# Kernel tuning notes

Measured on AMD Instinct MI355X. Metric: run time of the kernel, lower is better.

The kernel has to match this reference:

```python
import jax, jax.numpy as jnp
import numpy as np

B, T, IN, HID, NC = 1024, 128, 512, 1024, 10

def setup_inputs() -> dict:
    key = jax.random.key(0)
    ks = jax.random.split(key, 4)
    x = jax.random.normal(ks[0], (B, T, IN), dtype=jnp.float32)
    Wxh = jax.random.normal(ks[1], (IN, HID), dtype=jnp.float32) * (1.0 / np.sqrt(IN))
    b_xh = jnp.zeros((HID,), dtype=jnp.float32)
    Whh = jax.random.normal(ks[2], (HID, HID), dtype=jnp.float32) * (1.0 / np.sqrt(HID))
    b_hh = jnp.zeros((HID,), dtype=jnp.float32)
    Why = jax.random.normal(ks[3], (HID, NC), dtype=jnp.float32) * (1.0 / np.sqrt(HID))
    b_y = jnp.zeros((NC,), dtype=jnp.float32)
    return {"x": x, "Wxh": Wxh, "b_xh": b_xh, "Whh": Whh, "b_hh": b_hh, "Why": Why, "b_y": b_y}

def reference(x, Wxh, b_xh, Whh, b_hh, Why, b_y):
    # Precompute input projections for all timesteps in one big GEMM: [B,T,HID]
    xproj = jnp.einsum('bti,ih->bth', x, Wxh) + b_xh
    h0 = jnp.zeros((x.shape[0], Whh.shape[0]), dtype=x.dtype)
    def step(h, xp_t):
        h = jnp.tanh(xp_t + h @ Whh + b_hh)
        return h, None
    hT, _ = jax.lax.scan(step, h0, jnp.swapaxes(xproj, 0, 1))  # scan over T
    return hT @ Why + b_y
```

## Files before the change

### kernel.cpp

```cpp
#include <hip/hip_runtime.h>
#include <hip/hip_bf16.h>

#define TT    128
#define BATCH 1024
#define INDIM 512
#define HIDD  1024
#define NCLS  10

typedef __bf16 bf16x8 __attribute__((ext_vector_type(8)));
typedef float  f32x4  __attribute__((ext_vector_type(4)));
typedef unsigned short u16x8 __attribute__((ext_vector_type(8)));

__device__ __forceinline__ unsigned short bf16b(float f) {
    __hip_bfloat16 h = __float2bfloat16(f);
    return __builtin_bit_cast(unsigned short, h);
}

__device__ __forceinline__ float tanh_fast(float x) {
    float e = __expf(2.0f * x);
    return 1.0f - 2.0f * __builtin_amdgcn_rcpf(e + 1.0f);
}

#define WAITV(n) asm volatile("s_waitcnt vmcnt(" #n ")" ::: "memory")
#define BAR()    asm volatile("s_barrier" ::: "memory")

__global__ __launch_bounds__(256) void prep_kernel(
    const float* __restrict__ Whh, const float* __restrict__ Wxh,
    __hip_bfloat16* __restrict__ WhhT_hi, __hip_bfloat16* __restrict__ WhhT_lo,
    __hip_bfloat16* __restrict__ WxhT_hi, __hip_bfloat16* __restrict__ WxhT_lo)
{
    __shared__ float tl[64][68];
    int bid = blockIdx.x, tid = threadIdx.x;
    const float* src; int N, k0, n0, dstride;
    __hip_bfloat16 *dhi, *dlo;
    if (bid < 256) { src = Whh; N = 1024; k0 = (bid >> 4) << 6; n0 = (bid & 15) << 6;
                     dhi = WhhT_hi; dlo = WhhT_lo; dstride = 1024; }
    else { int b = bid - 256; src = Wxh; N = 1024; k0 = (b >> 4) << 6; n0 = (b & 15) << 6;
           dhi = WxhT_hi; dlo = WxhT_lo; dstride = 512; }

    int r = tid >> 2, c0 = (tid & 3) << 4;
    const float* s = src + (size_t)(k0 + r) * N + n0 + c0;
#pragma unroll
    for (int j = 0; j < 4; ++j)
        *(float4*)&tl[r][c0 + j * 4] = *(const float4*)(s + j * 4);
    __syncthreads();

    int rn = tid >> 2, ck0 = (tid & 3) << 4;
    u16x8 hi0, hi1, lo0, lo1;
#pragma unroll
    for (int j = 0; j < 16; ++j) {
        float w = tl[ck0 + j][rn];
        unsigned short hb = bf16b(w);
        float hf = __bfloat162float(__builtin_bit_cast(__hip_bfloat16, hb));
        unsigned short lb = bf16b(w - hf);
        if (j < 8) { hi0[j] = hb; lo0[j] = lb; }
        else       { hi1[j - 8] = hb; lo1[j - 8] = lb; }
    }
    size_t o = (size_t)(n0 + rn) * dstride + k0 + ck0;
    *(u16x8*)(void*)(dhi + o)     = hi0;
    *(u16x8*)(void*)(dhi + o + 8) = hi1;
    *(u16x8*)(void*)(dlo + o)     = lo0;
    *(u16x8*)(void*)(dlo + o + 8) = lo1;
}

__global__ __launch_bounds__(256) void convx_all_kernel(
    const float* __restrict__ x, __hip_bfloat16* __restrict__ xs)
{
    size_t gid = (size_t)blockIdx.x * 256 + threadIdx.x;
    int i  = (int)(gid & 63) << 3;
    size_t bt = gid >> 6;
    int t = (int)(bt & 127);
    int b = (int)(bt >> 7);
    const float* s = x + ((size_t)b * TT + t) * INDIM + i;
    float4 a0 = *(const float4*)s, a1 = *(const float4*)(s + 4);
    u16x8 o;
    o[0]=bf16b(a0.x); o[1]=bf16b(a0.y); o[2]=bf16b(a0.z); o[3]=bf16b(a0.w);
    o[4]=bf16b(a1.x); o[5]=bf16b(a1.y); o[6]=bf16b(a1.z); o[7]=bf16b(a1.w);
    *(u16x8*)(void*)(xs + ((size_t)t * BATCH + b) * INDIM + i) = o;
}

__global__ __launch_bounds__(256) void zero_kernel(
    __hip_bfloat16* __restrict__ h, unsigned* __restrict__ bar)
{
    if (blockIdx.x < 512) {
        size_t i = ((size_t)blockIdx.x * 256 + threadIdx.x) << 3;
        u16x8 z = {0,0,0,0,0,0,0,0};
        *(u16x8*)(void*)(h + i) = z;
    } else {
        uint4 z = {0,0,0,0};
#pragma unroll
        for (int k = 0; k < 8; ++k)
            ((uint4*)bar)[k * 256 + threadIdx.x] = z;
    }
}

#define FRAGA(_b, m, ks) \
    (*(const bf16x8*)((_b) + ((((m)<<4)+ar) << 8) + ((((((ks)<<2)+kg)) ^ (ar & 7)) << 4)))

#define STAGE(basePtr, rs, bufidx, AUX) do {                                   \
    _Pragma("unroll")                                                          \
    for (int _i = 0; _i < 4; ++_i) {                                           \
        int _r = (_i << 4) + (tid >> 4);                                       \
        int _s = (tid & 15) ^ (_r & 7);                                        \
        const void* _g = (const void*)((basePtr) + (size_t)_r * (rs) + (_s << 3)); \
        void* _l = (void*)(smem + ((bufidx) << 14) + (_i << 12) + (wave << 10));   \
        __builtin_amdgcn_global_load_lds(                                      \
            (const __attribute__((address_space(1))) void*)_g,                 \
            (__attribute__((address_space(3))) void*)_l, 16, 0, AUX);          \
    } } while (0)

#define DO_CHUNK(B_ARR, q, bufidx) do {                                        \
    const char* _b = smem + ((bufidx) << 14);                                  \
    _Pragma("unroll")                                                          \
    for (int ks = 0; ks < 4; ++ks) {                                           \
        bf16x8 a0 = FRAGA(_b, 0, ks), a1 = FRAGA(_b, 1, ks);                   \
        bf16x8 a2 = FRAGA(_b, 2, ks), a3 = FRAGA(_b, 3, ks);                   \
        bf16x8 bh = B_ARR[(q)*8+ks*2+0], bl = B_ARR[(q)*8+ks*2+1];             \
        acc0 = __builtin_amdgcn_mfma_f32_16x16x32_bf16(a0, bh, acc0, 0,0,0);   \
        acc1 = __builtin_amdgcn_mfma_f32_16x16x32_bf16(a1, bh, acc1, 0,0,0);   \
        acc2 = __builtin_amdgcn_mfma_f32_16x16x32_bf16(a2, bh, acc2, 0,0,0);   \
        acc3 = __builtin_amdgcn_mfma_f32_16x16x32_bf16(a3, bh, acc3, 0,0,0);   \
        acc0 = __builtin_amdgcn_mfma_f32_16x16x32_bf16(a0, bl, acc0, 0,0,0);   \
        acc1 = __builtin_amdgcn_mfma_f32_16x16x32_bf16(a1, bl, acc1, 0,0,0);   \
        acc2 = __builtin_amdgcn_mfma_f32_16x16x32_bf16(a2, bl, acc2, 0,0,0);   \
        acc3 = __builtin_amdgcn_mfma_f32_16x16x32_bf16(a3, bl, acc3, 0,0,0);   \
    } } while (0)

__global__ __launch_bounds__(256, 1) void rnn_kernel(
    __hip_bfloat16* __restrict__ h0, __hip_bfloat16* __restrict__ h1,
    const __hip_bfloat16* __restrict__ xs,
    const __hip_bfloat16* __restrict__ WhhT_hi, const __hip_bfloat16* __restrict__ WhhT_lo,
    const __hip_bfloat16* __restrict__ WxhT_hi, const __hip_bfloat16* __restrict__ WxhT_lo,
    const float* __restrict__ b_xh, const float* __restrict__ b_hh,
    unsigned* __restrict__ bar)
{
    __shared__ char smem[131072];
    int tid = threadIdx.x, bid = blockIdx.x;
    int by = (bid & 7) | (((bid >> 3) & 1) << 3);
    int bx = bid >> 4;
    int lane = tid & 63, wave = tid >> 6;
    int ar = lane & 15, kg = lane >> 4;
    int wcol = (bx << 6) + (wave << 4);
    int by64 = by << 6;

    bf16x8 Bh[64], Bx[32];
    {
        const __hip_bfloat16* hiB = WhhT_hi + (size_t)(wcol + ar) * HIDD + (kg << 3);
        const __hip_bfloat16* loB = WhhT_lo + (size_t)(wcol + ar) * HIDD + (kg << 3);
#pragma unroll
        for (int c = 0; c < 8; ++c)
#pragma unroll
            for (int ks = 0; ks < 4; ++ks) {
                Bh[c*8 + ks*2 + 0] = *(const bf16x8*)(hiB + c*128 + ks*32);
                Bh[c*8 + ks*2 + 1] = *(const bf16x8*)(loB + c*128 + ks*32);
            }
        const __hip_bfloat16* hiX = WxhT_hi + (size_t)(wcol + ar) * INDIM + (kg << 3);
        const __hip_bfloat16* loX = WxhT_lo + (size_t)(wcol + ar) * INDIM + (kg << 3);
#pragma unroll
        for (int c = 0; c < 4; ++c)
#pragma unroll
            for (int ks = 0; ks < 4; ++ks) {
                Bx[c*8 + ks*2 + 0] = *(const bf16x8*)(hiX + c*128 + ks*32);
                Bx[c*8 + ks*2 + 1] = *(const bf16x8*)(loX + c*128 + ks*32);
            }
    }
    int mycol = wcol + ar;
    float bias = b_xh[mycol] + b_hh[mycol];

    unsigned* grpflags = bar + (by << 9);
    unsigned* myflag   = grpflags + (bx << 5);

    {
        const __hip_bfloat16* xA0 = xs + (size_t)by64 * INDIM;
        STAGE(xA0 + 0*128, INDIM, 2, 0);
        STAGE(xA0 + 1*128, INDIM, 3, 0);
        STAGE(xA0 + 2*128, INDIM, 0, 0);
        STAGE(xA0 + 3*128, INDIM, 1, 0);
    }
    WAITV(0); BAR();

    for (int t = 0; t < TT; ++t) {
        const __hip_bfloat16* hA = (t & 1) ? h1 : h0;
        __hip_bfloat16*       hB = (t & 1) ? h0 : h1;
        const __hip_bfloat16* hR = hA + (size_t)by64 * HIDD;
        const __hip_bfloat16* xN = xs + (size_t)(t + 1) * (BATCH * INDIM)
                                      + (size_t)by64 * INDIM;
        int nl = (t < TT - 1);

        f32x4 acc0 = {0,0,0,0}, acc1 = {0,0,0,0}, acc2 = {0,0,0,0}, acc3 = {0,0,0,0};

        DO_CHUNK(Bx, 0, 2);
        DO_CHUNK(Bx, 1, 3);
        DO_CHUNK(Bx, 2, 0);
        DO_CHUNK(Bx, 3, 1);

        if (t > 0) {
            if (wave == 0) {
                unsigned tgt = (unsigned)t;
                for (;;) {
                    unsigned v = tgt;
                    if (lane < 16)
                        v = __hip_atomic_load(grpflags + (lane << 5), __ATOMIC_RELAXED,
                                              __HIP_MEMORY_SCOPE_SYSTEM);
                    if (__all(v >= tgt)) break;
                    __builtin_amdgcn_s_sleep(1);
                }
            }
        }
        BAR();

        STAGE(hR + 0*128, HIDD, 4, 1);
        STAGE(hR + 1*128, HIDD, 5, 1);
        STAGE(hR + 2*128, HIDD, 6, 1);
        STAGE(hR + 3*128, HIDD, 7, 1);
        STAGE(hR + 4*128, HIDD, 0, 1);
        STAGE(hR + 5*128, HIDD, 1, 1);
        if (nl) {
            STAGE(xN + 0*128, INDIM, 2, 0);
            STAGE(xN + 1*128, INDIM, 3, 0);
            WAITV(16);
        } else {
            WAITV(8);
        }
        BAR();
        DO_CHUNK(Bh, 0, 4);
        DO_CHUNK(Bh, 1, 5);
        DO_CHUNK(Bh, 2, 6);
        DO_CHUNK(Bh, 3, 7);
        if (nl) { WAITV(8); } else { WAITV(0); }
        BAR();
        STAGE(hR + 6*128, HIDD, 6, 1);
        STAGE(hR + 7*128, HIDD, 7, 1);
        DO_CHUNK(Bh, 4, 0);
        DO_CHUNK(Bh, 5, 1);
        WAITV(0);
        BAR();
        if (nl) {
            STAGE(xN + 2*128, INDIM, 0, 0);
            STAGE(xN + 3*128, INDIM, 1, 0);
        }
        DO_CHUNK(Bh, 6, 6);
        DO_CHUNK(Bh, 7, 7);

#pragma unroll
        for (int m = 0; m < 4; ++m) {
            f32x4 a = (m == 0) ? acc0 : (m == 1) ? acc1 : (m == 2) ? acc2 : acc3;
#pragma unroll
            for (int j = 0; j < 4; ++j) {
                int row = by64 + (m << 4) + (kg << 2) + j;
                float v = tanh_fast(a[j] + bias);
                hB[(size_t)row * HIDD + mycol] = __float2bfloat16(v);
            }
        }
        WAITV(0);
        BAR();
        if (nl && tid == 0)
            __hip_atomic_store(myflag, (unsigned)(t + 1), __ATOMIC_RELAXED,
                               __HIP_MEMORY_SCOPE_SYSTEM);
    }
}

__global__ __launch_bounds__(64) void out_kernel(
    const __hip_bfloat16* __restrict__ h, const float* __restrict__ Why,
    const float* __restrict__ b_y, float* __restrict__ out)
{
    int b = blockIdx.x, lane = threadIdx.x;
    float acc[NCLS];
#pragma unroll
    for (int c = 0; c < NCLS; ++c) acc[c] = 0.f;
    for (int kk = 0; kk < 16; ++kk) {
        int k = (kk << 6) + lane;
        float hv = __bfloat162float(h[(size_t)b * HIDD + k]);
#pragma unroll
        for (int c = 0; c < NCLS; ++c) acc[c] += hv * Why[(size_t)k * NCLS + c];
    }
#pragma unroll
    for (int c = 0; c < NCLS; ++c) {
        float v = acc[c];
#pragma unroll
        for (int off = 32; off > 0; off >>= 1) v += __shfl_down(v, off);
        if (lane == 0) out[(size_t)b * NCLS + c] = v + b_y[c];
    }
}

extern "C" void kernel_launch(void* const* d_in, const int* in_sizes, int n_in,
                              void* d_out, int out_size, void* d_ws, size_t ws_size,
                              hipStream_t stream)
{
    const float* x    = (const float*)d_in[0];
    const float* Wxh  = (const float*)d_in[1];
    const float* b_xh = (const float*)d_in[2];
    const float* Whh  = (const float*)d_in[3];
    const float* b_hh = (const float*)d_in[4];
    const float* Why  = (const float*)d_in[5];
    const float* b_y  = (const float*)d_in[6];
    float* out = (float*)d_out;

    char* ws = (char*)d_ws;
    __hip_bfloat16* WhhT_hi = (__hip_bfloat16*)(ws);
    __hip_bfloat16* WhhT_lo = (__hip_bfloat16*)(ws + (2u  << 20));
    __hip_bfloat16* WxhT_hi = (__hip_bfloat16*)(ws + (4u  << 20));
    __hip_bfloat16* WxhT_lo = (__hip_bfloat16*)(ws + (5u  << 20));
    __hip_bfloat16* h0      = (__hip_bfloat16*)(ws + (6u  << 20));
    __hip_bfloat16* h1      = (__hip_bfloat16*)(ws + (8u  << 20));
    unsigned*       bar     = (unsigned*)      (ws + (10u << 20));
    __hip_bfloat16* xs      = (__hip_bfloat16*)(ws + (16u << 20));

    prep_kernel<<<384, 256, 0, stream>>>(Whh, Wxh, WhhT_hi, WhhT_lo, WxhT_hi, WxhT_lo);
    convx_all_kernel<<<32768, 256, 0, stream>>>(x, xs);
    zero_kernel<<<513, 256, 0, stream>>>(h0, bar);

    rnn_kernel<<<256, 256, 0, stream>>>(h0, h1, xs,
                                        WhhT_hi, WhhT_lo, WxhT_hi, WxhT_lo,
                                        b_xh, b_hh, bar);

    out_kernel<<<1024, 64, 0, stream>>>(h0, Why, b_y, out);
}
```

Baseline: 881.1 us.

## Replace full-group barrier wait with per-chunk flag polling in rotated K order

Each block used to wait for all 16 producer blocks of its row group before staging any of the previous hidden state. Now every wave polls only the two producer flags covering the next 128-column K chunk before staging that chunk. Blocks start at a rotated chunk offset (bx>>1), with the Whh register fragments loaded in the same rotated order, so blocks spread their dependencies and can start as soon as part of h is ready. Flag scope is also narrowed from system to agent. The cost is more polling spread across all waves and more atomic loads, and the correctness of the relaxed ordering between flags and h data depends on existing fences.

Measured after the change: 1.035 ms. +17.5%, slower.

```diff
diff --git a/kernel.cpp b/kernel.cpp
--- a/kernel.cpp
+++ b/kernel.cpp
@@ -126,6 +126,13 @@
         acc3 = __builtin_amdgcn_mfma_f32_16x16x32_bf16(a3, bl, acc3, 0,0,0);   \
     } } while (0)
 
+#define POLL(c_) do { if (t > 0) {                                             \
+    unsigned _s = (((unsigned)(c_)) << 1) | (lane & 1);                        \
+    while (!__all(__hip_atomic_load(grpflags + (_s << 5), __ATOMIC_RELAXED,    \
+                                    __HIP_MEMORY_SCOPE_AGENT) >= (unsigned)t)) \
+        __builtin_amdgcn_s_sleep(1);                                           \
+} } while (0)
+
 __global__ __launch_bounds__(256, 1) void rnn_kernel(
     __hip_bfloat16* __restrict__ h0, __hip_bfloat16* __restrict__ h1,
     const __hip_bfloat16* __restrict__ xs,
@@ -142,18 +149,21 @@
     int ar = lane & 15, kg = lane >> 4;
     int wcol = (bx << 6) + (wave << 4);
     int by64 = by << 6;
+    int rb = bx >> 1;
 
     bf16x8 Bh[64], Bx[32];
     {
         const __hip_bfloat16* hiB = WhhT_hi + (size_t)(wcol + ar) * HIDD + (kg << 3);
         const __hip_bfloat16* loB = WhhT_lo + (size_t)(wcol + ar) * HIDD + (kg << 3);
 #pragma unroll
-        for (int c = 0; c < 8; ++c)
+        for (int c = 0; c < 8; ++c) {
+            int cc = (rb + c) & 7;
 #pragma unroll
             for (int ks = 0; ks < 4; ++ks) {
-                Bh[c*8 + ks*2 + 0] = *(const bf16x8*)(hiB + c*128 + ks*32);
-                Bh[c*8 + ks*2 + 1] = *(const bf16x8*)(loB + c*128 + ks*32);
+                Bh[c*8 + ks*2 + 0] = *(const bf16x8*)(hiB + cc*128 + ks*32);
+                Bh[c*8 + ks*2 + 1] = *(const bf16x8*)(loB + cc*128 + ks*32);
             }
+        }
         const __hip_bfloat16* hiX = WxhT_hi + (size_t)(wcol + ar) * INDIM + (kg << 3);
         const __hip_bfloat16* loX = WxhT_lo + (size_t)(wcol + ar) * INDIM + (kg << 3);
 #pragma unroll
@@ -193,28 +203,14 @@
         DO_CHUNK(Bx, 1, 3);
         DO_CHUNK(Bx, 2, 0);
         DO_CHUNK(Bx, 3, 1);
-
-        if (t > 0) {
-            if (wave == 0) {
-                unsigned tgt = (unsigned)t;
-                for (;;) {
-                    unsigned v = tgt;
-                    if (lane < 16)
-                        v = __hip_atomic_load(grpflags + (lane << 5), __ATOMIC_RELAXED,
-                                              __HIP_MEMORY_SCOPE_SYSTEM);
-                    if (__all(v >= tgt)) break;
-                    __builtin_amdgcn_s_sleep(1);
-                }
-            }
-        }
-        BAR();
-
-        STAGE(hR + 0*128, HIDD, 4, 1);
-        STAGE(hR + 1*128, HIDD, 5, 1);
-        STAGE(hR + 2*128, HIDD, 6, 1);
-        STAGE(hR + 3*128, HIDD, 7, 1);
-        STAGE(hR + 4*128, HIDD, 0, 1);
-        STAGE(hR + 5*128, HIDD, 1, 1);
+        BAR();
+
+        POLL((rb + 0) & 7); STAGE(hR + (size_t)(((rb + 0) & 7) << 7), HIDD, 4, 1);
+        POLL((rb + 1) & 7); STAGE(hR + (size_t)(((rb + 1) & 7) << 7), HIDD, 5, 1);
+        POLL((rb + 2) & 7); STAGE(hR + (size_t)(((rb + 2) & 7) << 7), HIDD, 6, 1);
+        POLL((rb + 3) & 7); STAGE(hR + (size_t)(((rb + 3) & 7) << 7), HIDD, 7, 1);
+        POLL((rb + 4) & 7); STAGE(hR + (size_t)(((rb + 4) & 7) << 7), HIDD, 0, 1);
+        POLL((rb + 5) & 7); STAGE(hR + (size_t)(((rb + 5) & 7) << 7), HIDD, 1, 1);
         if (nl) {
             STAGE(xN + 0*128, INDIM, 2, 0);
             STAGE(xN + 1*128, INDIM, 3, 0);
@@ -229,8 +225,8 @@
         DO_CHUNK(Bh, 3, 7);
         if (nl) { WAITV(8); } else { WAITV(0); }
         BAR();
-        STAGE(hR + 6*128, HIDD, 6, 1);
-        STAGE(hR + 7*128, HIDD, 7, 1);
+        POLL((rb + 6) & 7); STAGE(hR + (size_t)(((rb + 6) & 7) << 7), HIDD, 6, 1);
+        POLL((rb + 7) & 7); STAGE(hR + (size_t)(((rb + 7) & 7) << 7), HIDD, 7, 1);
         DO_CHUNK(Bh, 4, 0);
         DO_CHUNK(Bh, 5, 1);
         WAITV(0);
@@ -256,7 +252,7 @@
         BAR();
         if (nl && tid == 0)
             __hip_atomic_store(myflag, (unsigned)(t + 1), __ATOMIC_RELAXED,
-                               __HIP_MEMORY_SCOPE_SYSTEM);
+                               __HIP_MEMORY_SCOPE_AGENT);
     }
 }
 
```

## Split K across waves with per-wave LDS staging and LDS reduction

Applied to the files above, without the earlier changes.

Each wave now owns a quarter of the K dimension for all 64 output columns, instead of a 16-column slice over the full K. Each wave stages its own A tiles into a private LDS region, so the block barriers inside the step are replaced by per-wave vmcnt waits. Partial sums are reduced through LDS at the end of each step. Every wave now polls the flags, and the flag scope drops from system to agent. This trades the block-wide barriers for an extra LDS reduction pass and four times as many accumulator registers.

New measurement: 1.262 ms. 1.43x slower.

```diff
diff --git a/kernel.cpp b/kernel.cpp
--- a/kernel.cpp
+++ b/kernel.cpp
@@ -22,6 +22,7 @@
 }
 
 #define WAITV(n) asm volatile("s_waitcnt vmcnt(" #n ")" ::: "memory")
+#define WAITL()  asm volatile("s_waitcnt lgkmcnt(0)" ::: "memory")
 #define BAR()    asm volatile("s_barrier" ::: "memory")
 
 __global__ __launch_bounds__(256) void prep_kernel(
@@ -94,36 +95,40 @@
     }
 }
 
-#define FRAGA(_b, m, ks) \
-    (*(const bf16x8*)((_b) + ((((m)<<4)+ar) << 8) + ((((((ks)<<2)+kg)) ^ (ar & 7)) << 4)))
-
-#define STAGE(basePtr, rs, bufidx, AUX) do {                                   \
+#define FRAGA64(_b, m, ks) \
+    (*(const bf16x8*)((_b) + ((((m)<<4)+ar) << 7) + (((((ks)<<2)+kg) ^ (ar & 7)) << 4)))
+
+#define STAGEW(basePtr, rs, bufptr, AUX) do {                                  \
     _Pragma("unroll")                                                          \
-    for (int _i = 0; _i < 4; ++_i) {                                           \
-        int _r = (_i << 4) + (tid >> 4);                                       \
-        int _s = (tid & 15) ^ (_r & 7);                                        \
-        const void* _g = (const void*)((basePtr) + (size_t)_r * (rs) + (_s << 3)); \
-        void* _l = (void*)(smem + ((bufidx) << 14) + (_i << 12) + (wave << 10));   \
+    for (int _i = 0; _i < 8; ++_i) {                                           \
+        const void* _g = (const void*)((basePtr) + (size_t)((_i<<3) + l3) * (rs) + se); \
+        void* _l = (void*)((bufptr) + (_i << 10));                             \
         __builtin_amdgcn_global_load_lds(                                      \
             (const __attribute__((address_space(1))) void*)_g,                 \
             (__attribute__((address_space(3))) void*)_l, 16, 0, AUX);          \
     } } while (0)
 
-#define DO_CHUNK(B_ARR, q, bufidx) do {                                        \
-    const char* _b = smem + ((bufidx) << 14);                                  \
+#define DO_CHUNK64(B_ARR, qb, bufptr) do {                                     \
     _Pragma("unroll")                                                          \
-    for (int ks = 0; ks < 4; ++ks) {                                           \
-        bf16x8 a0 = FRAGA(_b, 0, ks), a1 = FRAGA(_b, 1, ks);                   \
-        bf16x8 a2 = FRAGA(_b, 2, ks), a3 = FRAGA(_b, 3, ks);                   \
-        bf16x8 bh = B_ARR[(q)*8+ks*2+0], bl = B_ARR[(q)*8+ks*2+1];             \
-        acc0 = __builtin_amdgcn_mfma_f32_16x16x32_bf16(a0, bh, acc0, 0,0,0);   \
-        acc1 = __builtin_amdgcn_mfma_f32_16x16x32_bf16(a1, bh, acc1, 0,0,0);   \
-        acc2 = __builtin_amdgcn_mfma_f32_16x16x32_bf16(a2, bh, acc2, 0,0,0);   \
-        acc3 = __builtin_amdgcn_mfma_f32_16x16x32_bf16(a3, bh, acc3, 0,0,0);   \
-        acc0 = __builtin_amdgcn_mfma_f32_16x16x32_bf16(a0, bl, acc0, 0,0,0);   \
-        acc1 = __builtin_amdgcn_mfma_f32_16x16x32_bf16(a1, bl, acc1, 0,0,0);   \
-        acc2 = __builtin_amdgcn_mfma_f32_16x16x32_bf16(a2, bl, acc2, 0,0,0);   \
-        acc3 = __builtin_amdgcn_mfma_f32_16x16x32_bf16(a3, bl, acc3, 0,0,0);   \
+    for (int _ks = 0; _ks < 2; ++_ks) {                                        \
+        bf16x8 a0 = FRAGA64(bufptr, 0, _ks), a1 = FRAGA64(bufptr, 1, _ks);     \
+        bf16x8 a2 = FRAGA64(bufptr, 2, _ks), a3 = FRAGA64(bufptr, 3, _ks);     \
+        _Pragma("unroll")                                                      \
+        for (int _cg = 0; _cg < 4; ++_cg) {                                    \
+            bf16x8 bh = B_ARR[((qb)+_ks)*8 + _cg*2 + 0];                       \
+            acc[0][_cg] = __builtin_amdgcn_mfma_f32_16x16x32_bf16(a0, bh, acc[0][_cg], 0,0,0); \
+            acc[1][_cg] = __builtin_amdgcn_mfma_f32_16x16x32_bf16(a1, bh, acc[1][_cg], 0,0,0); \
+            acc[2][_cg] = __builtin_amdgcn_mfma_f32_16x16x32_bf16(a2, bh, acc[2][_cg], 0,0,0); \
+            acc[3][_cg] = __builtin_amdgcn_mfma_f32_16x16x32_bf16(a3, bh, acc[3][_cg], 0,0,0); \
+        }                                                                      \
+        _Pragma("unroll")                                                      \
+        for (int _cg = 0; _cg < 4; ++_cg) {                                    \
+            bf16x8 bl = B_ARR[((qb)+_ks)*8 + _cg*2 + 1];                       \
+            acc[0][_cg] = __builtin_amdgcn_mfma_f32_16x16x32_bf16(a0, bl, acc[0][_cg], 0,0,0); \
+            acc[1][_cg] = __builtin_amdgcn_mfma_f32_16x16x32_bf16(a1, bl, acc[1][_cg], 0,0,0); \
+            acc[2][_cg] = __builtin_amdgcn_mfma_f32_16x16x32_bf16(a2, bl, acc[2][_cg], 0,0,0); \
+            acc[3][_cg] = __builtin_amdgcn_mfma_f32_16x16x32_bf16(a3, bl, acc[3][_cg], 0,0,0); \
+        }                                                                      \
     } } while (0)
 
 __global__ __launch_bounds__(256, 1) void rnn_kernel(
@@ -138,125 +143,127 @@
     int tid = threadIdx.x, bid = blockIdx.x;
     int by = (bid & 7) | (((bid >> 3) & 1) << 3);
     int bx = bid >> 4;
-    int lane = tid & 63, wave = tid >> 6;
+    int lane = tid & 63, w = tid >> 6;
     int ar = lane & 15, kg = lane >> 4;
-    int wcol = (bx << 6) + (wave << 4);
-    int by64 = by << 6;
+    int l3 = lane >> 3;
+    int se = ((lane & 7) ^ l3) << 3;
+    int bx64 = bx << 6, by64 = by << 6;
+    char* wb = smem + (w << 15);
 
     bf16x8 Bh[64], Bx[32];
-    {
-        const __hip_bfloat16* hiB = WhhT_hi + (size_t)(wcol + ar) * HIDD + (kg << 3);
-        const __hip_bfloat16* loB = WhhT_lo + (size_t)(wcol + ar) * HIDD + (kg << 3);
-#pragma unroll
-        for (int c = 0; c < 8; ++c)
-#pragma unroll
-            for (int ks = 0; ks < 4; ++ks) {
-                Bh[c*8 + ks*2 + 0] = *(const bf16x8*)(hiB + c*128 + ks*32);
-                Bh[c*8 + ks*2 + 1] = *(const bf16x8*)(loB + c*128 + ks*32);
-            }
-        const __hip_bfloat16* hiX = WxhT_hi + (size_t)(wcol + ar) * INDIM + (kg << 3);
-        const __hip_bfloat16* loX = WxhT_lo + (size_t)(wcol + ar) * INDIM + (kg << 3);
-#pragma unroll
-        for (int c = 0; c < 4; ++c)
-#pragma unroll
-            for (int ks = 0; ks < 4; ++ks) {
-                Bx[c*8 + ks*2 + 0] = *(const bf16x8*)(hiX + c*128 + ks*32);
-                Bx[c*8 + ks*2 + 1] = *(const bf16x8*)(loX + c*128 + ks*32);
-            }
-    }
-    int mycol = wcol + ar;
-    float bias = b_xh[mycol] + b_hh[mycol];
+    float bias[4];
+#pragma unroll
+    for (int cg = 0; cg < 4; ++cg) {
+        int col = bx64 + (cg << 4) + ar;
+        bias[cg] = b_xh[col] + b_hh[col];
+#pragma unroll
+        for (int kc = 0; kc < 8; ++kc) {
+            int k = (w << 8) + (kc << 5) + (kg << 3);
+            Bh[kc*8 + cg*2 + 0] = *(const bf16x8*)(WhhT_hi + (size_t)col * HIDD + k);
+            Bh[kc*8 + cg*2 + 1] = *(const bf16x8*)(WhhT_lo + (size_t)col * HIDD + k);
+        }
+#pragma unroll
+        for (int kc = 0; kc < 4; ++kc) {
+            int k = (w << 7) + (kc << 5) + (kg << 3);
+            Bx[kc*8 + cg*2 + 0] = *(const bf16x8*)(WxhT_hi + (size_t)col * INDIM + k);
+            Bx[kc*8 + cg*2 + 1] = *(const bf16x8*)(WxhT_lo + (size_t)col * INDIM + k);
+        }
+    }
 
     unsigned* grpflags = bar + (by << 9);
     unsigned* myflag   = grpflags + (bx << 5);
 
     {
-        const __hip_bfloat16* xA0 = xs + (size_t)by64 * INDIM;
-        STAGE(xA0 + 0*128, INDIM, 2, 0);
-        STAGE(xA0 + 1*128, INDIM, 3, 0);
-        STAGE(xA0 + 2*128, INDIM, 0, 0);
-        STAGE(xA0 + 3*128, INDIM, 1, 0);
-    }
-    WAITV(0); BAR();
+        const __hip_bfloat16* xA0 = xs + (size_t)by64 * INDIM + (w << 7);
+        STAGEW(xA0,      INDIM, wb + (2 << 13), 0);
+        STAGEW(xA0 + 64, INDIM, wb + (3 << 13), 0);
+    }
 
     for (int t = 0; t < TT; ++t) {
         const __hip_bfloat16* hA = (t & 1) ? h1 : h0;
         __hip_bfloat16*       hB = (t & 1) ? h0 : h1;
-        const __hip_bfloat16* hR = hA + (size_t)by64 * HIDD;
+        const __hip_bfloat16* hR = hA + (size_t)by64 * HIDD + (w << 8);
         const __hip_bfloat16* xN = xs + (size_t)(t + 1) * (BATCH * INDIM)
-                                      + (size_t)by64 * INDIM;
+                                      + (size_t)by64 * INDIM + (w << 7);
         int nl = (t < TT - 1);
-
-        f32x4 acc0 = {0,0,0,0}, acc1 = {0,0,0,0}, acc2 = {0,0,0,0}, acc3 = {0,0,0,0};
-
-        DO_CHUNK(Bx, 0, 2);
-        DO_CHUNK(Bx, 1, 3);
-        DO_CHUNK(Bx, 2, 0);
-        DO_CHUNK(Bx, 3, 1);
-
-        if (t > 0) {
-            if (wave == 0) {
-                unsigned tgt = (unsigned)t;
-                for (;;) {
-                    unsigned v = tgt;
-                    if (lane < 16)
-                        v = __hip_atomic_load(grpflags + (lane << 5), __ATOMIC_RELAXED,
-                                              __HIP_MEMORY_SCOPE_SYSTEM);
-                    if (__all(v >= tgt)) break;
-                    __builtin_amdgcn_s_sleep(1);
-                }
+        int xsel = (t & 1) ? 0 : 2;
+        char* bX0 = wb + (xsel << 13);
+        char* bX1 = bX0 + 8192;
+        char* bH0 = wb + ((xsel ^ 2) << 13);
+        char* bH1 = bH0 + 8192;
+
+        f32x4 acc[4][4];
+#pragma unroll
+        for (int m = 0; m < 4; ++m)
+#pragma unroll
+            for (int cg = 0; cg < 4; ++cg) acc[m][cg] = (f32x4){0,0,0,0};
+
+        WAITV(8);  DO_CHUNK64(Bx, 0, bX0);
+        WAITV(0);  DO_CHUNK64(Bx, 2, bX1);
+
+        {
+            unsigned tgt = (unsigned)t;
+            const unsigned* fp = grpflags + (((w << 2) + (lane & 3)) << 5);
+            for (;;) {
+                unsigned v = __hip_atomic_load(fp, __ATOMIC_RELAXED,
+                                               __HIP_MEMORY_SCOPE_AGENT);
+                if (__all(v >= tgt)) break;
+                __builtin_amdgcn_s_sleep(1);
             }
         }
-        BAR();
-
-        STAGE(hR + 0*128, HIDD, 4, 1);
-        STAGE(hR + 1*128, HIDD, 5, 1);
-        STAGE(hR + 2*128, HIDD, 6, 1);
-        STAGE(hR + 3*128, HIDD, 7, 1);
-        STAGE(hR + 4*128, HIDD, 0, 1);
-        STAGE(hR + 5*128, HIDD, 1, 1);
+
+        STAGEW(hR,       HIDD, bH0, 1);
+        STAGEW(hR +  64, HIDD, bH1, 1);
+        STAGEW(hR + 128, HIDD, bX0, 1);
+        STAGEW(hR + 192, HIDD, bX1, 1);
+        WAITV(24); DO_CHUNK64(Bh, 0, bH0);
+        WAITV(16); DO_CHUNK64(Bh, 2, bH1);
         if (nl) {
-            STAGE(xN + 0*128, INDIM, 2, 0);
-            STAGE(xN + 1*128, INDIM, 3, 0);
-            WAITV(16);
+            STAGEW(xN,      INDIM, bH0, 0);
+            STAGEW(xN + 64, INDIM, bH1, 0);
+            WAITV(24); DO_CHUNK64(Bh, 4, bX0);
+            WAITV(16); DO_CHUNK64(Bh, 6, bX1);
         } else {
-            WAITV(8);
-        }
-        BAR();
-        DO_CHUNK(Bh, 0, 4);
-        DO_CHUNK(Bh, 1, 5);
-        DO_CHUNK(Bh, 2, 6);
-        DO_CHUNK(Bh, 3, 7);
-        if (nl) { WAITV(8); } else { WAITV(0); }
-        BAR();
-        STAGE(hR + 6*128, HIDD, 6, 1);
-        STAGE(hR + 7*128, HIDD, 7, 1);
-        DO_CHUNK(Bh, 4, 0);
-        DO_CHUNK(Bh, 5, 1);
-        WAITV(0);
-        BAR();
-        if (nl) {
-            STAGE(xN + 2*128, INDIM, 0, 0);
-            STAGE(xN + 3*128, INDIM, 1, 0);
-        }
-        DO_CHUNK(Bh, 6, 6);
-        DO_CHUNK(Bh, 7, 7);
-
-#pragma unroll
-        for (int m = 0; m < 4; ++m) {
-            f32x4 a = (m == 0) ? acc0 : (m == 1) ? acc1 : (m == 2) ? acc2 : acc3;
+            WAITV(8);  DO_CHUNK64(Bh, 4, bX0);
+            WAITV(0);  DO_CHUNK64(Bh, 6, bX1);
+        }
+
+        {
+            char* pr = wb + (xsel << 13);
+#pragma unroll
+            for (int m = 0; m < 4; ++m)
+#pragma unroll
+                for (int cg = 0; cg < 4; ++cg)
+                    *(f32x4*)(pr + (((m << 2) + cg) << 10) + (lane << 4)) = acc[m][cg];
+        }
+        WAITL(); BAR();
+
+        f32x4 s0 = {0,0,0,0}, s1 = {0,0,0,0}, s2 = {0,0,0,0}, s3 = {0,0,0,0};
+#pragma unroll
+        for (int v = 0; v < 4; ++v) {
+            const char* prv = smem + (v << 15) + (xsel << 13) + ((w << 2) << 10) + (lane << 4);
+            s0 += *(const f32x4*)(prv);
+            s1 += *(const f32x4*)(prv + 1024);
+            s2 += *(const f32x4*)(prv + 2048);
+            s3 += *(const f32x4*)(prv + 3072);
+        }
+
+#pragma unroll
+        for (int cg = 0; cg < 4; ++cg) {
+            f32x4 sv = (cg == 0) ? s0 : (cg == 1) ? s1 : (cg == 2) ? s2 : s3;
+            int col = bx64 + (cg << 4) + ar;
+            float bs = bias[cg];
 #pragma unroll
             for (int j = 0; j < 4; ++j) {
-                int row = by64 + (m << 4) + (kg << 2) + j;
-                float v = tanh_fast(a[j] + bias);
-                hB[(size_t)row * HIDD + mycol] = __float2bfloat16(v);
+                int row = by64 + (w << 4) + (kg << 2) + j;
+                hB[(size_t)row * HIDD + col] = __float2bfloat16(tanh_fast(sv[j] + bs));
             }
         }
         WAITV(0);
         BAR();
         if (nl && tid == 0)
             __hip_atomic_store(myflag, (unsigned)(t + 1), __ATOMIC_RELAXED,
-                               __HIP_MEMORY_SCOPE_SYSTEM);
+                               __HIP_MEMORY_SCOPE_AGENT);
     }
 }
 
```

## Split K across wave pairs with 32-column tiles and LDS partial-sum reduction

Applied to the files above, without the earlier changes.

Each wave now computes 32 output columns over half of the K dimension instead of 16 columns over the full K. Every A fragment read from LDS is therefore reused by twice as many MFMAs, and the two K-halves are summed through a new LDS scratch buffer before tanh and the store. The LDS buffer schedule for h and x staging is reorganised around a ninth 16KB buffer. The flag atomics move from system scope to agent scope. This cuts LDS read traffic per MFMA, at the cost of an extra barrier and a reduction round-trip through LDS each timestep.

Result: slower. 2.778 ms (+215.3%).

```diff
diff --git a/kernel.cpp b/kernel.cpp
--- a/kernel.cpp
+++ b/kernel.cpp
@@ -22,6 +22,7 @@
 }
 
 #define WAITV(n) asm volatile("s_waitcnt vmcnt(" #n ")" ::: "memory")
+#define WAITL()  asm volatile("s_waitcnt lgkmcnt(0)" ::: "memory")
 #define BAR()    asm volatile("s_barrier" ::: "memory")
 
 __global__ __launch_bounds__(256) void prep_kernel(
@@ -94,6 +95,8 @@
     }
 }
 
+#define BUF(i) (smem + ((i) << 14))
+
 #define FRAGA(_b, m, ks) \
     (*(const bf16x8*)((_b) + ((((m)<<4)+ar) << 8) + ((((((ks)<<2)+kg)) ^ (ar & 7)) << 4)))
 
@@ -109,21 +112,23 @@
             (__attribute__((address_space(3))) void*)_l, 16, 0, AUX);          \
     } } while (0)
 
-#define DO_CHUNK(B_ARR, q, bufidx) do {                                        \
-    const char* _b = smem + ((bufidx) << 14);                                  \
+#define MF(a_, b_, c_) c_ = __builtin_amdgcn_mfma_f32_16x16x32_bf16(a_, b_, c_, 0,0,0)
+#define DO_CHUNK(B_ARR, q, bufptr) do {                                        \
+    const char* _b = (const char*)(bufptr);                                    \
     _Pragma("unroll")                                                          \
-    for (int ks = 0; ks < 4; ++ks) {                                           \
-        bf16x8 a0 = FRAGA(_b, 0, ks), a1 = FRAGA(_b, 1, ks);                   \
-        bf16x8 a2 = FRAGA(_b, 2, ks), a3 = FRAGA(_b, 3, ks);                   \
-        bf16x8 bh = B_ARR[(q)*8+ks*2+0], bl = B_ARR[(q)*8+ks*2+1];             \
-        acc0 = __builtin_amdgcn_mfma_f32_16x16x32_bf16(a0, bh, acc0, 0,0,0);   \
-        acc1 = __builtin_amdgcn_mfma_f32_16x16x32_bf16(a1, bh, acc1, 0,0,0);   \
-        acc2 = __builtin_amdgcn_mfma_f32_16x16x32_bf16(a2, bh, acc2, 0,0,0);   \
-        acc3 = __builtin_amdgcn_mfma_f32_16x16x32_bf16(a3, bh, acc3, 0,0,0);   \
-        acc0 = __builtin_amdgcn_mfma_f32_16x16x32_bf16(a0, bl, acc0, 0,0,0);   \
-        acc1 = __builtin_amdgcn_mfma_f32_16x16x32_bf16(a1, bl, acc1, 0,0,0);   \
-        acc2 = __builtin_amdgcn_mfma_f32_16x16x32_bf16(a2, bl, acc2, 0,0,0);   \
-        acc3 = __builtin_amdgcn_mfma_f32_16x16x32_bf16(a3, bl, acc3, 0,0,0);   \
+    for (int _ks = 0; _ks < 4; ++_ks) {                                        \
+        bf16x8 a0 = FRAGA(_b, 0, _ks), a1 = FRAGA(_b, 1, _ks);                 \
+        bf16x8 a2 = FRAGA(_b, 2, _ks), a3 = FRAGA(_b, 3, _ks);                 \
+        bf16x8 b00 = B_ARR[(q)*16 + _ks*4 + 0], b01 = B_ARR[(q)*16 + _ks*4 + 2]; \
+        bf16x8 b10 = B_ARR[(q)*16 + _ks*4 + 1], b11 = B_ARR[(q)*16 + _ks*4 + 3]; \
+        MF(a0, b00, acc[0][0]); MF(a1, b00, acc[1][0]);                        \
+        MF(a2, b00, acc[2][0]); MF(a3, b00, acc[3][0]);                        \
+        MF(a0, b01, acc[0][1]); MF(a1, b01, acc[1][1]);                        \
+        MF(a2, b01, acc[2][1]); MF(a3, b01, acc[3][1]);                        \
+        MF(a0, b10, acc[0][0]); MF(a1, b10, acc[1][0]);                        \
+        MF(a2, b10, acc[2][0]); MF(a3, b10, acc[3][0]);                        \
+        MF(a0, b11, acc[0][1]); MF(a1, b11, acc[1][1]);                        \
+        MF(a2, b11, acc[2][1]); MF(a3, b11, acc[3][1]);                        \
     } } while (0)
 
 __global__ __launch_bounds__(256, 1) void rnn_kernel(
@@ -134,48 +139,48 @@
     const float* __restrict__ b_xh, const float* __restrict__ b_hh,
     unsigned* __restrict__ bar)
 {
-    __shared__ char smem[131072];
+    __shared__ char smem[147456];
     int tid = threadIdx.x, bid = blockIdx.x;
     int by = (bid & 7) | (((bid >> 3) & 1) << 3);
     int bx = bid >> 4;
     int lane = tid & 63, wave = tid >> 6;
+    int kh = wave & 1, nh = wave >> 1;
     int ar = lane & 15, kg = lane >> 4;
-    int wcol = (bx << 6) + (wave << 4);
-    int by64 = by << 6;
+    int bx64 = bx << 6, by64 = by << 6;
 
     bf16x8 Bh[64], Bx[32];
-    {
-        const __hip_bfloat16* hiB = WhhT_hi + (size_t)(wcol + ar) * HIDD + (kg << 3);
-        const __hip_bfloat16* loB = WhhT_lo + (size_t)(wcol + ar) * HIDD + (kg << 3);
-#pragma unroll
-        for (int c = 0; c < 8; ++c)
+    float bias[2];
+#pragma unroll
+    for (int cg = 0; cg < 2; ++cg) {
+        int col = bx64 + (nh << 5) + (cg << 4) + ar;
+        bias[cg] = b_xh[col] + b_hh[col];
+#pragma unroll
+        for (int q = 0; q < 4; ++q)
 #pragma unroll
             for (int ks = 0; ks < 4; ++ks) {
-                Bh[c*8 + ks*2 + 0] = *(const bf16x8*)(hiB + c*128 + ks*32);
-                Bh[c*8 + ks*2 + 1] = *(const bf16x8*)(loB + c*128 + ks*32);
+                int k = (((kh << 2) + q) << 7) + (ks << 5) + (kg << 3);
+                Bh[q*16 + ks*4 + cg*2 + 0] = *(const bf16x8*)(WhhT_hi + (size_t)col * HIDD + k);
+                Bh[q*16 + ks*4 + cg*2 + 1] = *(const bf16x8*)(WhhT_lo + (size_t)col * HIDD + k);
             }
-        const __hip_bfloat16* hiX = WxhT_hi + (size_t)(wcol + ar) * INDIM + (kg << 3);
-        const __hip_bfloat16* loX = WxhT_lo + (size_t)(wcol + ar) * INDIM + (kg << 3);
-#pragma unroll
-        for (int c = 0; c < 4; ++c)
+#pragma unroll
+        for (int q = 0; q < 2; ++q)
 #pragma unroll
             for (int ks = 0; ks < 4; ++ks) {
-                Bx[c*8 + ks*2 + 0] = *(const bf16x8*)(hiX + c*128 + ks*32);
-                Bx[c*8 + ks*2 + 1] = *(const bf16x8*)(loX + c*128 + ks*32);
+                int k = (((kh << 1) + q) << 7) + (ks << 5) + (kg << 3);
+                Bx[q*16 + ks*4 + cg*2 + 0] = *(const bf16x8*)(WxhT_hi + (size_t)col * INDIM + k);
+                Bx[q*16 + ks*4 + cg*2 + 1] = *(const bf16x8*)(WxhT_lo + (size_t)col * INDIM + k);
             }
     }
-    int mycol = wcol + ar;
-    float bias = b_xh[mycol] + b_hh[mycol];
 
     unsigned* grpflags = bar + (by << 9);
     unsigned* myflag   = grpflags + (bx << 5);
 
     {
         const __hip_bfloat16* xA0 = xs + (size_t)by64 * INDIM;
-        STAGE(xA0 + 0*128, INDIM, 2, 0);
-        STAGE(xA0 + 1*128, INDIM, 3, 0);
-        STAGE(xA0 + 2*128, INDIM, 0, 0);
-        STAGE(xA0 + 3*128, INDIM, 1, 0);
+        STAGE(xA0 + 0*128, INDIM, 0, 0);
+        STAGE(xA0 + 1*128, INDIM, 1, 0);
+        STAGE(xA0 + 2*128, INDIM, 2, 0);
+        STAGE(xA0 + 3*128, INDIM, 3, 0);
     }
     WAITV(0); BAR();
 
@@ -187,76 +192,93 @@
                                       + (size_t)by64 * INDIM;
         int nl = (t < TT - 1);
 
-        f32x4 acc0 = {0,0,0,0}, acc1 = {0,0,0,0}, acc2 = {0,0,0,0}, acc3 = {0,0,0,0};
-
-        DO_CHUNK(Bx, 0, 2);
-        DO_CHUNK(Bx, 1, 3);
-        DO_CHUNK(Bx, 2, 0);
-        DO_CHUNK(Bx, 3, 1);
-
-        if (t > 0) {
-            if (wave == 0) {
-                unsigned tgt = (unsigned)t;
-                for (;;) {
-                    unsigned v = tgt;
-                    if (lane < 16)
-                        v = __hip_atomic_load(grpflags + (lane << 5), __ATOMIC_RELAXED,
-                                              __HIP_MEMORY_SCOPE_SYSTEM);
-                    if (__all(v >= tgt)) break;
-                    __builtin_amdgcn_s_sleep(1);
-                }
+        f32x4 acc[4][2];
+#pragma unroll
+        for (int m = 0; m < 4; ++m) { acc[m][0] = (f32x4){0,0,0,0}; acc[m][1] = (f32x4){0,0,0,0}; }
+
+        if (kh == 0) { DO_CHUNK(Bx, 0, BUF(0)); DO_CHUNK(Bx, 1, BUF(1)); }
+        else         { DO_CHUNK(Bx, 0, BUF(2)); DO_CHUNK(Bx, 1, BUF(3)); }
+
+        if (t > 0 && wave == 0) {
+            unsigned tgt = (unsigned)t;
+            for (;;) {
+                unsigned v = tgt;
+                if (lane < 16)
+                    v = __hip_atomic_load(grpflags + (lane << 5), __ATOMIC_RELAXED,
+                                          __HIP_MEMORY_SCOPE_AGENT);
+                if (__all(v >= tgt)) break;
+                __builtin_amdgcn_s_sleep(1);
             }
         }
         BAR();
 
         STAGE(hR + 0*128, HIDD, 4, 1);
         STAGE(hR + 1*128, HIDD, 5, 1);
-        STAGE(hR + 2*128, HIDD, 6, 1);
-        STAGE(hR + 3*128, HIDD, 7, 1);
-        STAGE(hR + 4*128, HIDD, 0, 1);
-        STAGE(hR + 5*128, HIDD, 1, 1);
+        STAGE(hR + 2*128, HIDD, 8, 1);
+        STAGE(hR + 4*128, HIDD, 6, 1);
+        STAGE(hR + 5*128, HIDD, 7, 1);
         if (nl) {
-            STAGE(xN + 0*128, INDIM, 2, 0);
-            STAGE(xN + 1*128, INDIM, 3, 0);
+            STAGE(xN + 0*128, INDIM, 0, 0);
+            STAGE(xN + 1*128, INDIM, 1, 0);
+            STAGE(xN + 2*128, INDIM, 2, 0);
+            STAGE(xN + 3*128, INDIM, 3, 0);
             WAITV(16);
         } else {
-            WAITV(8);
+            WAITV(0);
         }
         BAR();
-        DO_CHUNK(Bh, 0, 4);
-        DO_CHUNK(Bh, 1, 5);
-        DO_CHUNK(Bh, 2, 6);
-        DO_CHUNK(Bh, 3, 7);
-        if (nl) { WAITV(8); } else { WAITV(0); }
-        BAR();
+
+        if (kh == 0) { DO_CHUNK(Bh, 0, BUF(4)); DO_CHUNK(Bh, 1, BUF(5)); DO_CHUNK(Bh, 2, BUF(8)); }
+        else         { DO_CHUNK(Bh, 0, BUF(6)); DO_CHUNK(Bh, 1, BUF(7)); }
+        BAR();
+
+        STAGE(hR + 3*128, HIDD, 5, 1);
         STAGE(hR + 6*128, HIDD, 6, 1);
         STAGE(hR + 7*128, HIDD, 7, 1);
-        DO_CHUNK(Bh, 4, 0);
-        DO_CHUNK(Bh, 5, 1);
         WAITV(0);
         BAR();
-        if (nl) {
-            STAGE(xN + 2*128, INDIM, 0, 0);
-            STAGE(xN + 3*128, INDIM, 1, 0);
+
+        if (kh == 0) { DO_CHUNK(Bh, 3, BUF(5)); }
+        else         { DO_CHUNK(Bh, 2, BUF(6)); DO_CHUNK(Bh, 3, BUF(7)); }
+
+        {
+            char* pw = smem + (8 << 14) + (wave << 12);
+            int mo = kh ? 0 : 2;
+#pragma unroll
+            for (int s = 0; s < 2; ++s)
+#pragma unroll
+                for (int cg = 0; cg < 2; ++cg)
+                    *(f32x4*)(pw + (((s << 1) | cg) << 10) + (lane << 4)) = acc[mo + s][cg];
         }
-        DO_CHUNK(Bh, 6, 6);
-        DO_CHUNK(Bh, 7, 7);
-
-#pragma unroll
-        for (int m = 0; m < 4; ++m) {
-            f32x4 a = (m == 0) ? acc0 : (m == 1) ? acc1 : (m == 2) ? acc2 : acc3;
-#pragma unroll
-            for (int j = 0; j < 4; ++j) {
-                int row = by64 + (m << 4) + (kg << 2) + j;
-                float v = tanh_fast(a[j] + bias);
-                hB[(size_t)row * HIDD + mycol] = __float2bfloat16(v);
-            }
+        WAITL(); BAR();
+
+        {
+            const char* pr = smem + (8 << 14) + ((wave ^ 1) << 12);
+            int mk = kh ? 2 : 0;
+#pragma unroll
+            for (int s = 0; s < 2; ++s)
+#pragma unroll
+                for (int cg = 0; cg < 2; ++cg)
+                    acc[mk + s][cg] += *(const f32x4*)(pr + (((s << 1) | cg) << 10) + (lane << 4));
+
+#pragma unroll
+            for (int s = 0; s < 2; ++s)
+#pragma unroll
+                for (int cg = 0; cg < 2; ++cg) {
+                    int col = bx64 + (nh << 5) + (cg << 4) + ar;
+                    f32x4 a = acc[mk + s][cg];
+#pragma unroll
+                    for (int j = 0; j < 4; ++j) {
+                        int row = by64 + ((mk + s) << 4) + (kg << 2) + j;
+                        hB[(size_t)row * HIDD + col] = __float2bfloat16(tanh_fast(a[j] + bias[cg]));
+                    }
+                }
         }
         WAITV(0);
         BAR();
         if (nl && tid == 0)
             __hip_atomic_store(myflag, (unsigned)(t + 1), __ATOMIC_RELAXED,
-                               __HIP_MEMORY_SCOPE_SYSTEM);
+                               __HIP_MEMORY_SCOPE_AGENT);
     }
 }
 
```
